# Kernel optimization log

Hardware: AMD Instinct MI355X
Metric: run time of the kernel (lower is better)

The kernel has to match this reference:

```python
import jax, jax.numpy as jnp
import numpy as np


def setup_inputs() -> dict:
    key = jax.random.key(0)
    k1, k2, k3 = jax.random.split(key, 3)
    B, T, D = 8, 4096, 1024
    x0 = jax.random.normal(k1, (B, D), dtype=jnp.float32)
    a = jax.random.uniform(k2, (B, T, D), dtype=jnp.float32)  # decay in [0,1) for stability
    u = jax.random.normal(k3, (B, T, D), dtype=jnp.float32)
    return {"x0": x0, "a": a, "u": u}


def _linear_scan(x0, a, u):
    # x_t = a_t * x_{t-1} + u_t, t = 1..T (x_0 given)
    # Fold x0 into the first step so the associative scan handles it uniformly.
    u0 = u.at[:, 0, :].add(a[:, 0, :] * x0)

    def combine(c1, c2):
        a1, u1 = c1
        a2, u2 = c2
        return a1 * a2, a2 * u1 + u2

    _, x = jax.lax.associative_scan(combine, (a, u0), axis=1)
    return x  # [B, T, D]


def reference(x0, a, u):
    return _linear_scan(x0, a, u)
```

## Files before the change

kernel.cpp:

```cpp
#include <hip/hip_runtime.h>

#define BB 8
#define TT 4096
#define DD 1024
#define SS 128
#define TSEG (TT / SS)
#define STR (DD / 4)
#define CH 8

typedef float natf4 __attribute__((ext_vector_type(4)));

static __device__ __forceinline__ float4 ffma4(const float4 a, const float4 x,
                                               const float4 u) {
  return make_float4(fmaf(a.x, x.x, u.x), fmaf(a.y, x.y, u.y),
                     fmaf(a.z, x.z, u.z), fmaf(a.w, x.w, u.w));
}
static __device__ __forceinline__ float4 fmul4(const float4 a, const float4 b) {
  return make_float4(a.x * b.x, a.y * b.y, a.z * b.z, a.w * b.w);
}
static __device__ __forceinline__ void nt_store4(float4* p, const float4 v) {
  natf4 nv;
  nv.x = v.x; nv.y = v.y; nv.z = v.z; nv.w = v.w;
  __builtin_nontemporal_store(nv, (natf4*)p);
}

__global__ __launch_bounds__(256) void seg_reduce(
    const float* __restrict__ a, const float* __restrict__ u,
    float* __restrict__ wsA, float* __restrict__ wsU) {
  const int b = blockIdx.x >> 7;
  const int s = blockIdx.x & (SS - 1);
  const int d4 = threadIdx.x << 2;

  const size_t base = ((size_t)b * TT + (size_t)s * TSEG) * DD + d4;
  const float4* __restrict__ ap = (const float4*)(a + base);
  const float4* __restrict__ up = (const float4*)(u + base);

  float4 A = make_float4(1.f, 1.f, 1.f, 1.f);
  float4 U = make_float4(0.f, 0.f, 0.f, 0.f);

#pragma unroll 1
  for (int tb = 0; tb < TSEG; tb += CH) {
    float4 av[CH], uv[CH];
#pragma unroll
    for (int k = 0; k < CH; ++k) {
      av[k] = ap[(size_t)(tb + k) * STR];
      uv[k] = up[(size_t)(tb + k) * STR];
    }
#pragma unroll
    for (int k = 0; k < CH; ++k) {
      U = ffma4(av[k], U, uv[k]);
      A = fmul4(A, av[k]);
    }
  }

  const size_t w = ((size_t)b * SS + s) * DD + d4;
  *(float4*)(wsA + w) = A;
  *(float4*)(wsU + w) = U;
}

__global__ __launch_bounds__(256) void seg_scan(
    const float* __restrict__ x0, const float* __restrict__ wsA,
    const float* __restrict__ wsU, float* __restrict__ xstart) {
  __shared__ float ldsA[SS * 64];
  __shared__ float ldsU[SS * 64];
  __shared__ float wsumA[4][64];
  __shared__ float wsumU[4][64];

  const int b  = blockIdx.x >> 4;
  const int d0 = (blockIdx.x & 15) << 6;
  const int ch = threadIdx.x & 63;
  const int wv = threadIdx.x >> 6;

#pragma unroll 8
  for (int it = 0; it < SS / 4; ++it) {
    const int s = (it << 2) + wv;
    const size_t g = ((size_t)b * SS + s) * DD + d0 + ch;
    ldsA[s * 64 + ch] = wsA[g];
    ldsU[s * 64 + ch] = wsU[g];
  }
  __syncthreads();

  float Ac = 1.f, Uc = 0.f;
  const int s0 = wv * (SS / 4);
#pragma unroll 8
  for (int k = 0; k < SS / 4; ++k) {
    const float As = ldsA[(s0 + k) * 64 + ch];
    const float Us = ldsU[(s0 + k) * 64 + ch];
    Uc = fmaf(As, Uc, Us);
    Ac *= As;
  }
  wsumA[wv][ch] = Ac;
  wsumU[wv][ch] = Uc;
  __syncthreads();

  float x = x0[(size_t)b * DD + d0 + ch];
  for (int w2 = 0; w2 < wv; ++w2)
    x = fmaf(wsumA[w2][ch], x, wsumU[w2][ch]);

#pragma unroll 8
  for (int k = 0; k < SS / 4; ++k) {
    const int s = s0 + k;
    xstart[((size_t)b * SS + s) * DD + d0 + ch] = x;
    x = fmaf(ldsA[s * 64 + ch], x, ldsU[s * 64 + ch]);
  }
}

__global__ __launch_bounds__(256) void seg_apply(
    const float* __restrict__ a, const float* __restrict__ u,
    const float* __restrict__ xstart, float* __restrict__ out) {
  const int b = blockIdx.x >> 7;
  const int s = blockIdx.x & (SS - 1);
  const int d4 = threadIdx.x << 2;

  const size_t base = ((size_t)b * TT + (size_t)s * TSEG) * DD + d4;
  const float4* __restrict__ ap = (const float4*)(a + base);
  const float4* __restrict__ up = (const float4*)(u + base);
  float4* __restrict__ op = (float4*)(out + base);

  const size_t w = ((size_t)b * SS + s) * DD + d4;
  float4 x = *(const float4*)(xstart + w);

#pragma unroll 1
  for (int tb = 0; tb < TSEG; tb += CH) {
    float4 av[CH], uv[CH];
#pragma unroll
    for (int k = 0; k < CH; ++k) {
      av[k] = ap[(size_t)(tb + k) * STR];
      uv[k] = up[(size_t)(tb + k) * STR];
    }
#pragma unroll
    for (int k = 0; k < CH; ++k) {
      x = ffma4(av[k], x, uv[k]);
      nt_store4(op + (size_t)(tb + k) * STR, x);
    }
  }
}

extern "C" void kernel_launch(void* const* d_in, const int* in_sizes, int n_in,
                              void* d_out, int out_size, void* d_ws, size_t ws_size,
                              hipStream_t stream) {
  const float* x0 = (const float*)d_in[0];
  const float* a  = (const float*)d_in[1];
  const float* u  = (const float*)d_in[2];
  float* out = (float*)d_out;

  const size_t seg_elems = (size_t)BB * SS * DD;
  float* wsA    = (float*)d_ws;
  float* wsU    = wsA + seg_elems;
  float* xstart = wsU + seg_elems;

  seg_reduce<<<BB * SS, 256, 0, stream>>>(a, u, wsA, wsU);
  seg_scan<<<BB * (DD / 64), 256, 0, stream>>>(x0, wsA, wsU, xstart);
  seg_apply<<<BB * SS, 256, 0, stream>>>(a, u, xstart, out);
}
```

Baseline: 364.5 us.

## Software-pipeline segment loads with inline asm double buffering and float2 lanes

The reduce and apply kernels move from float4 per thread with 256 threads to float2 per thread with 512 threads. Each kernel now issues hand-written global_load_dwordx2 into double-buffered registers and uses explicit s_waitcnt vmcnt counts, so the next chunk's loads are in flight while the current chunk is computed. The apply kernel also replaces the nontemporal stores with plain asm stores, and keeps the store data registers live until their stores retire. The aim is to hide memory latency and keep more bytes in flight. The costs are fragile hand-counted waitcnt values, the loss of the nontemporal store hint, and narrower memory accesses.

```diff
diff --git a/kernel.cpp b/kernel.cpp
--- a/kernel.cpp
+++ b/kernel.cpp
@@ -5,57 +5,67 @@
 #define DD 1024
 #define SS 128
 #define TSEG (TT / SS)
-#define STR (DD / 4)
-#define CH 8
+#define STR2 (DD / 2)
+#define CH 4
+#define NB (TSEG / CH)
 
-typedef float natf4 __attribute__((ext_vector_type(4)));
+typedef float natf2 __attribute__((ext_vector_type(2)));
 
-static __device__ __forceinline__ float4 ffma4(const float4 a, const float4 x,
-                                               const float4 u) {
-  return make_float4(fmaf(a.x, x.x, u.x), fmaf(a.y, x.y, u.y),
-                     fmaf(a.z, x.z, u.z), fmaf(a.w, x.w, u.w));
-}
-static __device__ __forceinline__ float4 fmul4(const float4 a, const float4 b) {
-  return make_float4(a.x * b.x, a.y * b.y, a.z * b.z, a.w * b.w);
-}
-static __device__ __forceinline__ void nt_store4(float4* p, const float4 v) {
-  natf4 nv;
-  nv.x = v.x; nv.y = v.y; nv.z = v.z; nv.w = v.w;
-  __builtin_nontemporal_store(nv, (natf4*)p);
-}
+#define GLOAD2(dst, ptr) \
+  asm volatile("global_load_dwordx2 %0, %1, off" : "=v"(dst) : "v"(ptr))
+#define GSTORE2(ptr, val) \
+  asm volatile("global_store_dwordx2 %0, %1, off" ::"v"(ptr), "v"(val) : "memory")
+#define SWAITV(n) asm volatile("s_waitcnt vmcnt(" #n ")" ::: "memory")
+#define KEEP(v) asm volatile("" ::"v"(v))
 
-__global__ __launch_bounds__(256) void seg_reduce(
+__global__ __launch_bounds__(512) void seg_reduce(
     const float* __restrict__ a, const float* __restrict__ u,
     float* __restrict__ wsA, float* __restrict__ wsU) {
   const int b = blockIdx.x >> 7;
   const int s = blockIdx.x & (SS - 1);
-  const int d4 = threadIdx.x << 2;
+  const int d2 = threadIdx.x << 1;
 
-  const size_t base = ((size_t)b * TT + (size_t)s * TSEG) * DD + d4;
-  const float4* __restrict__ ap = (const float4*)(a + base);
-  const float4* __restrict__ up = (const float4*)(u + base);
+  const size_t base = ((size_t)b * TT + (size_t)s * TSEG) * DD + d2;
+  const natf2* __restrict__ ap = (const natf2*)(a + base);
+  const natf2* __restrict__ up = (const natf2*)(u + base);
 
-  float4 A = make_float4(1.f, 1.f, 1.f, 1.f);
-  float4 U = make_float4(0.f, 0.f, 0.f, 0.f);
+  natf2 av[2][CH], uv[2][CH];
+#pragma unroll
+  for (int k = 0; k < CH; ++k) {
+    GLOAD2(av[0][k], ap + (size_t)k * STR2);
+    GLOAD2(uv[0][k], up + (size_t)k * STR2);
+  }
 
-#pragma unroll 1
-  for (int tb = 0; tb < TSEG; tb += CH) {
-    float4 av[CH], uv[CH];
+  natf2 A = {1.f, 1.f};
+  natf2 U = {0.f, 0.f};
+
+#pragma unroll
+  for (int i = 0; i < NB; ++i) {
+    const int pb = i & 1;
+    if (i + 1 < NB) {
+#pragma unroll
+      for (int k = 0; k < CH; ++k) {
+        GLOAD2(av[pb ^ 1][k], ap + (size_t)((i + 1) * CH + k) * STR2);
+        GLOAD2(uv[pb ^ 1][k], up + (size_t)((i + 1) * CH + k) * STR2);
+      }
+      SWAITV(8);
+    } else {
+      SWAITV(0);
+    }
+    __builtin_amdgcn_sched_barrier(0);
 #pragma unroll
     for (int k = 0; k < CH; ++k) {
-      av[k] = ap[(size_t)(tb + k) * STR];
-      uv[k] = up[(size_t)(tb + k) * STR];
-    }
-#pragma unroll
-    for (int k = 0; k < CH; ++k) {
-      U = ffma4(av[k], U, uv[k]);
-      A = fmul4(A, av[k]);
+      const natf2 a2 = av[pb][k], u2 = uv[pb][k];
+      U.x = fmaf(a2.x, U.x, u2.x);
+      U.y = fmaf(a2.y, U.y, u2.y);
+      A.x *= a2.x;
+      A.y *= a2.y;
     }
   }
 
-  const size_t w = ((size_t)b * SS + s) * DD + d4;
-  *(float4*)(wsA + w) = A;
-  *(float4*)(wsU + w) = U;
+  const size_t w = ((size_t)b * SS + s) * DD + d2;
+  *(natf2*)(wsA + w) = A;
+  *(natf2*)(wsU + w) = U;
 }
 
 __global__ __launch_bounds__(256) void seg_scan(
@@ -105,35 +115,58 @@
   }
 }
 
-__global__ __launch_bounds__(256) void seg_apply(
+__global__ __launch_bounds__(512) void seg_apply(
     const float* __restrict__ a, const float* __restrict__ u,
     const float* __restrict__ xstart, float* __restrict__ out) {
   const int b = blockIdx.x >> 7;
   const int s = blockIdx.x & (SS - 1);
-  const int d4 = threadIdx.x << 2;
+  const int d2 = threadIdx.x << 1;
 
-  const size_t base = ((size_t)b * TT + (size_t)s * TSEG) * DD + d4;
-  const float4* __restrict__ ap = (const float4*)(a + base);
-  const float4* __restrict__ up = (const float4*)(u + base);
-  float4* __restrict__ op = (float4*)(out + base);
+  const size_t base = ((size_t)b * TT + (size_t)s * TSEG) * DD + d2;
+  const natf2* __restrict__ ap = (const natf2*)(a + base);
+  const natf2* __restrict__ up = (const natf2*)(u + base);
+  natf2* __restrict__ op = (natf2*)(out + base);
 
-  const size_t w = ((size_t)b * SS + s) * DD + d4;
-  float4 x = *(const float4*)(xstart + w);
+  const size_t w = ((size_t)b * SS + s) * DD + d2;
+  natf2 x = *(const natf2*)(xstart + w);
 
-#pragma unroll 1
-  for (int tb = 0; tb < TSEG; tb += CH) {
-    float4 av[CH], uv[CH];
+  natf2 av[2][CH], uv[2][CH], sv[2][CH];
 #pragma unroll
-    for (int k = 0; k < CH; ++k) {
-      av[k] = ap[(size_t)(tb + k) * STR];
-      uv[k] = up[(size_t)(tb + k) * STR];
+  for (int k = 0; k < CH; ++k) {
+    GLOAD2(av[0][k], ap + (size_t)k * STR2);
+    GLOAD2(uv[0][k], up + (size_t)k * STR2);
+  }
+
+#pragma unroll
+  for (int i = 0; i < NB; ++i) {
+    const int pb = i & 1;
+    if (i + 1 < NB) {
+#pragma unroll
+      for (int k = 0; k < CH; ++k) {
+        GLOAD2(av[pb ^ 1][k], ap + (size_t)((i + 1) * CH + k) * STR2);
+        GLOAD2(uv[pb ^ 1][k], up + (size_t)((i + 1) * CH + k) * STR2);
+      }
+      if (i == 0) { SWAITV(8); } else { SWAITV(12); }
+    } else {
+      SWAITV(4);
+    }
+    __builtin_amdgcn_sched_barrier(0);
+    if (i >= 2) {
+#pragma unroll
+      for (int k = 0; k < CH; ++k) KEEP(sv[pb][k]);
     }
 #pragma unroll
     for (int k = 0; k < CH; ++k) {
-      x = ffma4(av[k], x, uv[k]);
-      nt_store4(op + (size_t)(tb + k) * STR, x);
+      const natf2 a2 = av[pb][k], u2 = uv[pb][k];
+      x.x = fmaf(a2.x, x.x, u2.x);
+      x.y = fmaf(a2.y, x.y, u2.y);
+      sv[pb][k] = x;
+      GSTORE2(op + (size_t)(i * CH + k) * STR2, sv[pb][k]);
     }
   }
+  SWAITV(0);
+#pragma unroll
+  for (int k = 0; k < CH; ++k) { KEEP(sv[0][k]); KEEP(sv[1][k]); }
 }
 
 extern "C" void kernel_launch(void* const* d_in, const int* in_sizes, int n_in,
@@ -149,7 +182,7 @@
   float* wsU    = wsA + seg_elems;
   float* xstart = wsU + seg_elems;
 
-  seg_reduce<<<BB * SS, 256, 0, stream>>>(a, u, wsA, wsU);
+  seg_reduce<<<BB * SS, 512, 0, stream>>>(a, u, wsA, wsU);
   seg_scan<<<BB * (DD / 64), 256, 0, stream>>>(x0, wsA, wsU, xstart);
-  seg_apply<<<BB * SS, 256, 0, stream>>>(a, u, xstart, out);
+  seg_apply<<<BB * SS, 512, 0, stream>>>(a, u, xstart, out);
 }
```

After: 387.1 us. 6.2% more time.
